# Kernel optimization log

Hardware: AMD Instinct MI355X
Metric: run time of the kernel (lower is better)

Reference implementation:

```python
import jax, jax.numpy as jnp
import numpy as np

B, NV, NH = 65536, 16, 16


def _tri(key, b, n, scale=0.1):
    # well-conditioned lower-triangular 'cholesky-like' factor: unit diagonal + small strict-lower part
    a = jax.random.normal(key, (b, n, n), dtype=jnp.float32) * scale
    return jnp.tril(a, -1) + jnp.eye(n, dtype=jnp.float32)[None, :, :]


def setup_inputs() -> dict:
    key = jax.random.key(0)
    ks = jax.random.split(key, 9)
    # SPD, well-conditioned precision matrix for the hidden block
    a = jax.random.normal(ks[0], (B, NH, NH), dtype=jnp.float32)
    prec_h = jnp.eye(NH, dtype=jnp.float32)[None, :, :] + 0.1 * jnp.matmul(a, jnp.swapaxes(a, -1, -2)) / NH
    return {
        'mu_TE': jax.random.normal(ks[1], (B, NV + NH), dtype=jnp.float32),
        'prec_h': prec_h,
        'chol_v': _tri(ks[2], B, NV),
        'chol_h': _tri(ks[3], B, NH),
        'chol_hv': jax.random.normal(ks[4], (B, NH, NV), dtype=jnp.float32) * 0.1,
        'chol_v_TE': jax.random.normal(ks[5], (B, NV, NV), dtype=jnp.float32) * 0.1,
        'chol_h_TE': jax.random.normal(ks[6], (B, NH, NH), dtype=jnp.float32) * 0.1,
        'chol_hv_TE': jax.random.normal(ks[7], (B, NH, NV), dtype=jnp.float32) * 0.1,
        'chol_amat': _tri(ks[8], B, NV),
        'nv': NV,
    }


def reference(mu_TE, prec_h, chol_v, chol_h, chol_hv, chol_v_TE, chol_h_TE, chol_hv_TE, chol_amat, nv):
    T = lambda m: jnp.swapaxes(m, -1, -2)
    prec_h_inv = jnp.linalg.inv(prec_h)  # [B,nh,nh]

    # d/dt of prec_h_inv via product rule on chol factors
    sym = (chol_h_TE @ T(chol_h) + chol_h @ T(chol_h_TE)
           + chol_hv_TE @ T(chol_hv) + chol_hv @ T(chol_hv_TE))
    prec_h_inv_TE = -(prec_h_inv @ sym @ prec_h_inv)

    # amat_TE = -d/dt [ chol_hv^T prec_h_inv chol_hv ]  -> [B,nv,nv]
    amat_TE = -(T(chol_hv_TE) @ (prec_h_inv @ chol_hv)
                + T(chol_hv) @ (prec_h_inv_TE @ chol_hv)
                + T(chol_hv) @ (prec_h_inv @ chol_hv_TE))

    # make_chol_mat_TE: Phi(L^-1 A L^-T) keeps strict lower triangle + half diagonal
    n = chol_amat.shape[-1]
    phi_mask = jnp.tril(jnp.ones((n, n), jnp.float32), -1) + 0.5 * jnp.eye(n, dtype=jnp.float32)
    cinv = jnp.linalg.inv(chol_amat)
    arg = cinv @ amat_TE @ T(cinv)
    chol_amat_TE = chol_amat @ (arg * phi_mask)

    cholv_TE_std = chol_v_TE @ chol_amat + chol_v @ chol_amat_TE
    muv_TE = mu_TE[:, :nv]
    return cholv_TE_std, muv_TE
```

## Files before the change

kernel.cpp:

```cpp
#include <hip/hip_runtime.h>


typedef _Float16 h2    __attribute__((ext_vector_type(2)));
typedef _Float16 f16x4 __attribute__((ext_vector_type(4)));
typedef float    f32x4 __attribute__((ext_vector_type(4)));

constexpr int PITCH = 20;
constexpr int IMG   = 8 * PITCH;
constexpr int BSTR  = 4 * IMG + 8;

#define WBAR() __builtin_amdgcn_wave_barrier()

__device__ __forceinline__ unsigned int pkf(float a, float b) {
  return __builtin_bit_cast(unsigned int, __builtin_amdgcn_cvt_pkrtz(a, b));
}
__device__ __forceinline__ f16x4 mkf16x4(unsigned int lo, unsigned int hi) {
  union { unsigned int u[2]; f16x4 v; } cv; cv.u[0] = lo; cv.u[1] = hi; return cv.v;
}
__device__ __forceinline__ f16x4 cvt4(f32x4 d) {
  return mkf16x4(pkf(d[0], d[1]), pkf(d[2], d[3]));
}
__device__ __forceinline__ f16x4 cvt4f(float a, float b, float c, float d) {
  return mkf16x4(pkf(a, b), pkf(c, d));
}
__device__ __forceinline__ float dpp_swap1(float v) {
  return __int_as_float(__builtin_amdgcn_update_dpp(
      0, __float_as_int(v), 0xB1, 0xF, 0xF, false));
}
__device__ __forceinline__ f32x4 MF(f16x4 a, f16x4 b, f32x4 c) {
  return __builtin_amdgcn_mfma_f32_16x16x16f16(a, b, c, 0, 0, 0);
}

__device__ __forceinline__ void ldtile(const float* __restrict__ g, size_t batch,
                                       int p, int q, float (&c)[16]) {
  const float* base = g + batch * 256 + p * 64 + q * 4;
  #pragma unroll
  for (int r = 0; r < 4; ++r) {
    float4 v = *reinterpret_cast<const float4*>(base + r * 16);
    c[r*4+0] = v.x; c[r*4+1] = v.y; c[r*4+2] = v.z; c[r*4+3] = v.w;
  }
}
__device__ __forceinline__ void storeRP(unsigned int* img, int p, int q, const float (&c)[16]) {
  #pragma unroll
  for (int r = 0; r < 4; ++r) {
    img[(2*q  ) * PITCH + 4*p + r] = pkf(c[r*4+0], c[r*4+1]);
    img[(2*q+1) * PITCH + 4*p + r] = pkf(c[r*4+2], c[r*4+3]);
  }
}
__device__ __forceinline__ void storeCPt(unsigned int* img, int p, int q, const float (&c)[16]) {
  uint4 w0, w1;
  w0.x = pkf(c[0],  c[4]);  w0.y = pkf(c[1],  c[5]);
  w0.z = pkf(c[2],  c[6]);  w0.w = pkf(c[3],  c[7]);
  w1.x = pkf(c[8],  c[12]); w1.y = pkf(c[9],  c[13]);
  w1.z = pkf(c[10], c[14]); w1.w = pkf(c[11], c[15]);
  *reinterpret_cast<uint4*>(img + (2*p  ) * PITCH + 4*q) = w0;
  *reinterpret_cast<uint4*>(img + (2*p+1) * PITCH + 4*q) = w1;
}

__device__ __forceinline__ f16x4 ldA(const float* __restrict__ X, int r, int h) {
  float4 v = *reinterpret_cast<const float4*>(X + r * 16 + 4 * h);
  return cvt4f(v.x, v.y, v.z, v.w);
}
__device__ __forceinline__ f16x4 ldBcol(const float* __restrict__ X, int h, int c) {
  const float* b = X + 4 * h * 16 + c;
  return cvt4f(b[0], b[16], b[32], b[48]);
}
__device__ __forceinline__ f16x4 ldsB(const unsigned int* img, int h, int c) {
  return mkf16x4(img[(2*h) * PITCH + c], img[(2*h+1) * PITCH + c]);
}
__device__ __forceinline__ f16x4 ldsA(const unsigned int* img, int r, int h) {
  uint4 u = *reinterpret_cast<const uint4*>(img + (r >> 1) * PITCH + 4 * h);
  unsigned int sel = 0x05040100u + (unsigned)(r & 1) * 0x02020202u;
  return mkf16x4(__builtin_amdgcn_perm(u.y, u.x, sel),
                 __builtin_amdgcn_perm(u.w, u.z, sel));
}
__device__ __forceinline__ void stCP(unsigned int* img, int h, int c, f32x4 d) {
  img[(2*h)   * PITCH + c] = pkf(d[0], d[1]);
  img[(2*h+1) * PITCH + c] = pkf(d[2], d[3]);
}

__global__ __launch_bounds__(64, 4) void gauss_te_mf(
    const float* __restrict__ mu_TE,
    const float* __restrict__ prec_h,
    const float* __restrict__ chol_v,
    const float* __restrict__ chol_h,
    const float* __restrict__ chol_hv,
    const float* __restrict__ chol_v_TE,
    const float* __restrict__ chol_h_TE,
    const float* __restrict__ chol_hv_TE,
    const float* __restrict__ chol_amat,
    float* __restrict__ out, int B)
{
  __shared__ __align__(16) unsigned int slab[4 * BSTR];
  const int t = threadIdx.x;
  const int g = t >> 4;
  const int l = t & 15;
  const int p = l >> 2, q = l & 3;
  const size_t batch0 = (size_t)blockIdx.x * 4;
  const size_t tb = batch0 + g;

  unsigned int* Ut  = slab + g * BSTR;
  unsigned int* Q0t = Ut;
  unsigned int* Q1t = Ut + IMG;
  unsigned int* Q2t = Ut + 2 * IMG;
  unsigned int* Q3t = Ut + 3 * IMG;
  float* fcol = reinterpret_cast<float*>(Q3t);
  float* brow = fcol + 32;

  out[(size_t)B * 256 + tb * 16 + l] = mu_TE[tb * 32 + l];

  f16x4 pfA0[4], pfB0[4], pfA1[4], pfB1[4];
  #pragma unroll
  for (int b = 0; b < 4; ++b) {
    const size_t off = (batch0 + b) * 256;
    pfA0[b] = ldA(chol_h_TE  + off, l, g);
    pfB0[b] = ldA(chol_h     + off, l, g);
    pfA1[b] = ldA(chol_hv_TE + off, l, g);
    pfB1[b] = ldA(chol_hv    + off, l, g);
  }

  float la[16];
  ldtile(chol_amat, tb, p, q, la);
  storeCPt(Q1t, p, q, la);
  float pt[16];
  ldtile(prec_h, tb, p, q, pt);
  WBAR();

  #pragma unroll
  for (int k = 0; k < 16; ++k) {
    const int kb = k >> 2, kc = k & 3, sel = (k & 1) * 16;
    if (q == kb) {
      *reinterpret_cast<float4*>(fcol + sel + 4 * p) =
          make_float4(pt[0*4+kc], pt[1*4+kc], pt[2*4+kc], pt[3*4+kc]);
    }
    WBAR();
    if (p == kb) {
      const float rinv = 1.0f / fcol[sel + k];
      float sv[4];
      #pragma unroll
      for (int j = 0; j < 4; ++j) sv[j] = pt[kc*4+j] * rinv;
      if (q == kb) sv[kc] = rinv;
      *reinterpret_cast<float4*>(brow + sel + 4 * q) = make_float4(sv[0], sv[1], sv[2], sv[3]);
    }
    WBAR();
    float4 f4 = *reinterpret_cast<const float4*>(fcol + sel + 4 * p);
    float4 b4 = *reinterpret_cast<const float4*>(brow + sel + 4 * q);
    const float fr[4] = {f4.x, f4.y, f4.z, f4.w};
    const float br[4] = {b4.x, b4.y, b4.z, b4.w};
    #pragma unroll
    for (int r = 0; r < 4; ++r) {
      const bool isPivRow = (p == kb) && (r == kc);
      #pragma unroll
      for (int j = 0; j < 4; ++j) {
        float base = pt[r*4+j];
        if (q == kb && j == kc) base = 0.f;
        const float nv = base - fr[r] * br[j];
        pt[r*4+j] = isPivRow ? br[j] : nv;
      }
    }
  }
  WBAR();
  storeRP(Q0t, p, q, pt);
  WBAR();

  float x[16];
  #pragma unroll
  for (int kp = 0; kp < 8; ++kp) {
    const int r0 = 2 * kp, r1 = r0 + 1;
    float a0 = 0.f, a1 = 0.f, h10 = 0.f;
    #pragma unroll
    for (int c2 = 0; c2 <= kp / 2; ++c2) {
      uint4 cv = *reinterpret_cast<const uint4*>(Q1t + kp * PITCH + 4 * c2);
      const unsigned int cw[4] = {cv.x, cv.y, cv.z, cv.w};
      #pragma unroll
      for (int cc = 0; cc < 4; ++cc) {
        const int j = 4 * c2 + cc;
        h2 hp = __builtin_bit_cast(h2, cw[cc]);
        if (j < r0) a0 = fmaf(-(float)hp.x, x[j], a0);
        if (j < r0) a1 = fmaf(-(float)hp.y, x[j], a1);
        if (j == r0) h10 = (float)hp.y;
      }
    }
    x[r0] = ((l == r0) ? 1.f : 0.f) + a0;
    x[r1] = ((l == r1) ? 1.f : 0.f) + a1 - h10 * x[r0];
  }
  {
    float xp[16];
    #pragma unroll
    for (int j = 0; j < 16; ++j) xp[j] = dpp_swap1(x[j]);
    if ((l & 1) == 0) {
      unsigned int* dst = Q2t + (l >> 1) * PITCH;
      #pragma unroll
      for (int c4 = 0; c4 < 4; ++c4) {
        uint4 w;
        w.x = pkf(x[4*c4+0], xp[4*c4+0]); w.y = pkf(x[4*c4+1], xp[4*c4+1]);
        w.z = pkf(x[4*c4+2], xp[4*c4+2]); w.w = pkf(x[4*c4+3], xp[4*c4+3]);
        *reinterpret_cast<uint4*>(dst + 4*c4) = w;
      }
    }
  }
  WBAR();

  const f32x4 zz = {0.f, 0.f, 0.f, 0.f};
  #pragma unroll
  for (int gb = 0; gb < 4; gb += 2) {
    const unsigned int* Q0[2] = { slab + (gb+0)*BSTR, slab + (gb+1)*BSTR };
    const unsigned int* Q1[2] = { Q0[0] + IMG,        Q0[1] + IMG };
    const unsigned int* Q2[2] = { Q0[0] + 2*IMG,      Q0[1] + 2*IMG };
    unsigned int*       Q3[2] = { slab + (gb+0)*BSTR + 3*IMG,
                                  slab + (gb+1)*BSTR + 3*IMG };
    const size_t off[2] = { (batch0 + gb + 0) * 256, (batch0 + gb + 1) * 256 };

    f16x4 pinvA[2], pinvB[2], hvB[2], cA[2], sumA[2];
    f32x4 W[2], M1[2], Up[2], Zt[2], V2[2];

    #pragma unroll
    for (int u = 0; u < 2; ++u) {
      f32x4 S = MF(pfA0[gb+u], pfB0[gb+u], zz);
      S = MF(pfA1[gb+u], pfB1[gb+u], S);
      pinvA[u] = ldsA(Q0[u], l, g);
      pinvB[u] = ldsB(Q0[u], g, l);
      f32x4 W1 = MF(pinvA[u], cvt4(S), zz);
      stCP(Q3[u], g, l, W1);
    }
    WBAR();
    #pragma unroll
    for (int u = 0; u < 2; ++u) {
      f16x4 w1A = ldsA(Q3[u], l, g);
      W[u] = MF(w1A, pinvB[u], zz);
    }
    #pragma unroll
    for (int u = 0; u < 2; ++u) stCP(Q3[u], g, l, W[u]);
    WBAR();
    #pragma unroll
    for (int u = 0; u < 2; ++u) {
      f16x4 wA = ldsA(Q3[u], l, g);
      sumA[u] = wA + cvt4(W[u]);
      hvB[u] = ldBcol(chol_hv + off[u], g, l);
      M1[u] = MF(pinvA[u], hvB[u], zz);
      Up[u] = MF(sumA[u], hvB[u], zz);
    }
    #pragma unroll
    for (int u = 0; u < 2; ++u) {
      f16x4 hvtB = ldBcol(chol_hv_TE + off[u], g, l);
      Zt[u] = MF(hvtB, cvt4(M1[u]), zz);
      V2[u] = MF(hvB[u], cvt4(Up[u]), zz);
      stCP(Q3[u], g, l, Zt[u]);
    }
    WBAR();
    f32x4 T1[2];
    #pragma unroll
    for (int u = 0; u < 2; ++u) {
      f16x4 zA = ldsA(Q3[u], l, g);
      f32x4 am = V2[u] - Zt[u];
      am[0] -= (float)zA[0]; am[1] -= (float)zA[1];
      am[2] -= (float)zA[2]; am[3] -= (float)zA[3];
      cA[u] = ldsB(Q2[u], g, l);
      T1[u] = MF(cA[u], cvt4(am), zz);
      stCP(Q3[u], g, l, T1[u]);
    }
    WBAR();
    #pragma unroll
    for (int u = 0; u < 2; ++u) {
      f16x4 t1A = ldsA(Q3[u], l, g);
      f32x4 arg = MF(t1A, cA[u], zz);
      #pragma unroll
      for (int j = 0; j < 4; ++j) {
        const int r = 4 * g + j;
        arg[j] = (r > l) ? arg[j] : ((r == l) ? 0.5f * arg[j] : 0.f);
      }
      f32x4 cam = MF(ldA(chol_amat + off[u], l, g), cvt4(arg), zz);
      f16x4 laB = ldsB(Q1[u], g, l);
      f32x4 ov = MF(ldA(chol_v_TE + off[u], l, g), laB, zz);
      ov = MF(ldA(chol_v + off[u], l, g), cvt4(cam), ov);
      float* ob = out + off[u];
      #pragma unroll
      for (int j = 0; j < 4; ++j) ob[(4 * g + j) * 16 + l] = ov[j];
    }
  }
}

extern "C" void kernel_launch(void* const* d_in, const int* in_sizes, int n_in,
                              void* d_out, int out_size, void* d_ws, size_t ws_size,
                              hipStream_t stream) {
  const float* mu_TE      = (const float*)d_in[0];
  const float* prec_h     = (const float*)d_in[1];
  const float* chol_v     = (const float*)d_in[2];
  const float* chol_h     = (const float*)d_in[3];
  const float* chol_hv    = (const float*)d_in[4];
  const float* chol_v_TE  = (const float*)d_in[5];
  const float* chol_h_TE  = (const float*)d_in[6];
  const float* chol_hv_TE = (const float*)d_in[7];
  const float* chol_amat  = (const float*)d_in[8];
  float* out = (float*)d_out;

  const int B = in_sizes[0] / 32;
  gauss_te_mf<<<B / 4, 64, 0, stream>>>(mu_TE, prec_h, chol_v, chol_h, chol_hv,
                                        chol_v_TE, chol_h_TE, chol_hv_TE,
                                        chol_amat, out, B);
}
```

Measured before the change: 126.6 us.

## Use DPP/swizzle Gauss-Jordan pivots and reassociate amat_TE chain to drop LDS round-trips

Result: faster. 122.0 us (-3.6%).

```diff
diff --git a/kernel.cpp b/kernel.cpp
--- a/kernel.cpp
+++ b/kernel.cpp
@@ -7,7 +7,7 @@
 
 constexpr int PITCH = 20;
 constexpr int IMG   = 8 * PITCH;
-constexpr int BSTR  = 4 * IMG + 8;
+constexpr int BSTR  = 3 * IMG + 8;
 
 #define WBAR() __builtin_amdgcn_wave_barrier()
 
@@ -29,6 +29,13 @@
 }
 __device__ __forceinline__ f32x4 MF(f16x4 a, f16x4 b, f32x4 c) {
   return __builtin_amdgcn_mfma_f32_16x16x16f16(a, b, c, 0, 0, 0);
+}
+__device__ __forceinline__ float frcp(float x) {
+#if __has_builtin(__builtin_amdgcn_rcpf)
+  return __builtin_amdgcn_rcpf(x);
+#else
+  return 1.0f / x;
+#endif
 }
 
 __device__ __forceinline__ void ldtile(const float* __restrict__ g, size_t batch,
@@ -79,7 +86,7 @@
   img[(2*h+1) * PITCH + c] = pkf(d[2], d[3]);
 }
 
-__global__ __launch_bounds__(64, 4) void gauss_te_mf(
+__global__ __launch_bounds__(64, 4) void gauss_te_mf2(
     const float* __restrict__ mu_TE,
     const float* __restrict__ prec_h,
     const float* __restrict__ chol_v,
@@ -103,9 +110,6 @@
   unsigned int* Q0t = Ut;
   unsigned int* Q1t = Ut + IMG;
   unsigned int* Q2t = Ut + 2 * IMG;
-  unsigned int* Q3t = Ut + 3 * IMG;
-  float* fcol = reinterpret_cast<float*>(Q3t);
-  float* brow = fcol + 32;
 
   out[(size_t)B * 256 + tb * 16 + l] = mu_TE[tb * 32 + l];
 
@@ -118,49 +122,49 @@
     pfA1[b] = ldA(chol_hv_TE + off, l, g);
     pfB1[b] = ldA(chol_hv    + off, l, g);
   }
+  float pt[16];
+  ldtile(prec_h, tb, p, q, pt);
+
+  #define GJ_STEP(K)                                                          \
+  {                                                                           \
+    constexpr int kb = (K) >> 2, kc = (K) & 3;                                \
+    float F[4];                                                               \
+    _Pragma("unroll")                                                         \
+    for (int r = 0; r < 4; ++r)                                               \
+      F[r] = __int_as_float(__builtin_amdgcn_update_dpp(                      \
+          0, __float_as_int(pt[r*4+kc]), kb * 0x55, 0xF, 0xF, false));        \
+    const float rinv = frcp(F[kc]);                                           \
+    float sv[4];                                                              \
+    _Pragma("unroll")                                                         \
+    for (int j = 0; j < 4; ++j) sv[j] = pt[kc*4+j] * rinv;                    \
+    if (q == kb) sv[kc] = rinv;                                               \
+    float br[4];                                                              \
+    _Pragma("unroll")                                                         \
+    for (int j = 0; j < 4; ++j)                                               \
+      br[j] = __int_as_float(__builtin_amdgcn_ds_swizzle(                     \
+          __float_as_int(sv[j]), ((kb << 2) << 5) | 0x13));                   \
+    _Pragma("unroll")                                                         \
+    for (int r = 0; r < 4; ++r) {                                             \
+      const bool isPivRow = (p == kb) && (r == kc);                           \
+      _Pragma("unroll")                                                       \
+      for (int j = 0; j < 4; ++j) {                                           \
+        float base = pt[r*4+j];                                               \
+        if (q == kb && j == kc) base = 0.f;                                   \
+        const float nv = base - F[r] * br[j];                                 \
+        pt[r*4+j] = isPivRow ? br[j] : nv;                                    \
+      }                                                                       \
+    }                                                                         \
+  }
+  GJ_STEP(0)  GJ_STEP(1)  GJ_STEP(2)  GJ_STEP(3)
+  GJ_STEP(4)  GJ_STEP(5)  GJ_STEP(6)  GJ_STEP(7)
+  GJ_STEP(8)  GJ_STEP(9)  GJ_STEP(10) GJ_STEP(11)
+  GJ_STEP(12) GJ_STEP(13) GJ_STEP(14) GJ_STEP(15)
+  #undef GJ_STEP
+  storeRP(Q0t, p, q, pt);
 
   float la[16];
   ldtile(chol_amat, tb, p, q, la);
   storeCPt(Q1t, p, q, la);
-  float pt[16];
-  ldtile(prec_h, tb, p, q, pt);
-  WBAR();
-
-  #pragma unroll
-  for (int k = 0; k < 16; ++k) {
-    const int kb = k >> 2, kc = k & 3, sel = (k & 1) * 16;
-    if (q == kb) {
-      *reinterpret_cast<float4*>(fcol + sel + 4 * p) =
-          make_float4(pt[0*4+kc], pt[1*4+kc], pt[2*4+kc], pt[3*4+kc]);
-    }
-    WBAR();
-    if (p == kb) {
-      const float rinv = 1.0f / fcol[sel + k];
-      float sv[4];
-      #pragma unroll
-      for (int j = 0; j < 4; ++j) sv[j] = pt[kc*4+j] * rinv;
-      if (q == kb) sv[kc] = rinv;
-      *reinterpret_cast<float4*>(brow + sel + 4 * q) = make_float4(sv[0], sv[1], sv[2], sv[3]);
-    }
-    WBAR();
-    float4 f4 = *reinterpret_cast<const float4*>(fcol + sel + 4 * p);
-    float4 b4 = *reinterpret_cast<const float4*>(brow + sel + 4 * q);
-    const float fr[4] = {f4.x, f4.y, f4.z, f4.w};
-    const float br[4] = {b4.x, b4.y, b4.z, b4.w};
-    #pragma unroll
-    for (int r = 0; r < 4; ++r) {
-      const bool isPivRow = (p == kb) && (r == kc);
-      #pragma unroll
-      for (int j = 0; j < 4; ++j) {
-        float base = pt[r*4+j];
-        if (q == kb && j == kc) base = 0.f;
-        const float nv = base - fr[r] * br[j];
-        pt[r*4+j] = isPivRow ? br[j] : nv;
-      }
-    }
-  }
-  WBAR();
-  storeRP(Q0t, p, q, pt);
   WBAR();
 
   float x[16];
@@ -204,65 +208,43 @@
   const f32x4 zz = {0.f, 0.f, 0.f, 0.f};
   #pragma unroll
   for (int gb = 0; gb < 4; gb += 2) {
-    const unsigned int* Q0[2] = { slab + (gb+0)*BSTR, slab + (gb+1)*BSTR };
-    const unsigned int* Q1[2] = { Q0[0] + IMG,        Q0[1] + IMG };
-    const unsigned int* Q2[2] = { Q0[0] + 2*IMG,      Q0[1] + 2*IMG };
-    unsigned int*       Q3[2] = { slab + (gb+0)*BSTR + 3*IMG,
-                                  slab + (gb+1)*BSTR + 3*IMG };
+    const unsigned int* Q1[2] = { slab + (gb+0)*BSTR + IMG,
+                                  slab + (gb+1)*BSTR + IMG };
+    const unsigned int* Q2[2] = { slab + (gb+0)*BSTR + 2*IMG,
+                                  slab + (gb+1)*BSTR + 2*IMG };
+    unsigned int*       Q0[2] = { slab + (gb+0)*BSTR, slab + (gb+1)*BSTR };
     const size_t off[2] = { (batch0 + gb + 0) * 256, (batch0 + gb + 1) * 256 };
 
-    f16x4 pinvA[2], pinvB[2], hvB[2], cA[2], sumA[2];
-    f32x4 W[2], M1[2], Up[2], Zt[2], V2[2];
-
+    f16x4 pinvF[2], hvB[2], hvtB[2], cA[2];
     #pragma unroll
     for (int u = 0; u < 2; ++u) {
-      f32x4 S = MF(pfA0[gb+u], pfB0[gb+u], zz);
-      S = MF(pfA1[gb+u], pfB1[gb+u], S);
-      pinvA[u] = ldsA(Q0[u], l, g);
-      pinvB[u] = ldsB(Q0[u], g, l);
-      f32x4 W1 = MF(pinvA[u], cvt4(S), zz);
-      stCP(Q3[u], g, l, W1);
+      hvB[u]  = ldBcol(chol_hv + off[u], g, l);
+      hvtB[u] = ldBcol(chol_hv_TE + off[u], g, l);
+      pinvF[u] = ldsA(Q0[u], l, g);
+      cA[u] = ldsB(Q2[u], g, l);
+    }
+    #pragma unroll
+    for (int u = 0; u < 2; ++u) {
+      f32x4 S  = MF(pfA0[gb+u], pfB0[gb+u], zz);
+      S        = MF(pfA1[gb+u], pfB1[gb+u], S);
+      f32x4 St = MF(pfB0[gb+u], pfA0[gb+u], zz);
+      St       = MF(pfB1[gb+u], pfA1[gb+u], St);
+      f32x4 sy = S + St;
+      f32x4 M1 = MF(pinvF[u], hvB[u], zz);
+      f16x4 m1h = cvt4(M1);
+      f32x4 G  = MF(cvt4(sy), m1h, zz);
+      f32x4 Up = MF(pinvF[u], cvt4(G), zz);
+      f32x4 Z  = MF(hvtB[u], m1h, zz);
+      f32x4 ZT = MF(m1h, hvtB[u], zz);
+      f32x4 V2 = MF(hvB[u], cvt4(Up), zz);
+      f32x4 am = V2 - Z - ZT;
+      f32x4 T1 = MF(cA[u], cvt4(am), zz);
+      stCP(Q0[u], g, l, T1);
     }
     WBAR();
     #pragma unroll
     for (int u = 0; u < 2; ++u) {
-      f16x4 w1A = ldsA(Q3[u], l, g);
-      W[u] = MF(w1A, pinvB[u], zz);
-    }
-    #pragma unroll
-    for (int u = 0; u < 2; ++u) stCP(Q3[u], g, l, W[u]);
-    WBAR();
-    #pragma unroll
-    for (int u = 0; u < 2; ++u) {
-      f16x4 wA = ldsA(Q3[u], l, g);
-      sumA[u] = wA + cvt4(W[u]);
-      hvB[u] = ldBcol(chol_hv + off[u], g, l);
-      M1[u] = MF(pinvA[u], hvB[u], zz);
-      Up[u] = MF(sumA[u], hvB[u], zz);
-    }
-    #pragma unroll
-    for (int u = 0; u < 2; ++u) {
-      f16x4 hvtB = ldBcol(chol_hv_TE + off[u], g, l);
-      Zt[u] = MF(hvtB, cvt4(M1[u]), zz);
-      V2[u] = MF(hvB[u], cvt4(Up[u]), zz);
-      stCP(Q3[u], g, l, Zt[u]);
-    }
-    WBAR();
-    f32x4 T1[2];
-    #pragma unroll
-    for (int u = 0; u < 2; ++u) {
-      f16x4 zA = ldsA(Q3[u], l, g);
-      f32x4 am = V2[u] - Zt[u];
-      am[0] -= (float)zA[0]; am[1] -= (float)zA[1];
-      am[2] -= (float)zA[2]; am[3] -= (float)zA[3];
-      cA[u] = ldsB(Q2[u], g, l);
-      T1[u] = MF(cA[u], cvt4(am), zz);
-      stCP(Q3[u], g, l, T1[u]);
-    }
-    WBAR();
-    #pragma unroll
-    for (int u = 0; u < 2; ++u) {
-      f16x4 t1A = ldsA(Q3[u], l, g);
+      f16x4 t1A = ldsA(Q0[u], l, g);
       f32x4 arg = MF(t1A, cA[u], zz);
       #pragma unroll
       for (int j = 0; j < 4; ++j) {
@@ -270,8 +252,7 @@
         arg[j] = (r > l) ? arg[j] : ((r == l) ? 0.5f * arg[j] : 0.f);
       }
       f32x4 cam = MF(ldA(chol_amat + off[u], l, g), cvt4(arg), zz);
-      f16x4 laB = ldsB(Q1[u], g, l);
-      f32x4 ov = MF(ldA(chol_v_TE + off[u], l, g), laB, zz);
+      f32x4 ov = MF(ldA(chol_v_TE + off[u], l, g), ldsB(Q1[u], g, l), zz);
       ov = MF(ldA(chol_v + off[u], l, g), cvt4(cam), ov);
       float* ob = out + off[u];
       #pragma unroll
@@ -295,7 +276,7 @@
   float* out = (float*)d_out;
 
   const int B = in_sizes[0] / 32;
-  gauss_te_mf<<<B / 4, 64, 0, stream>>>(mu_TE, prec_h, chol_v, chol_h, chol_hv,
-                                        chol_v_TE, chol_h_TE, chol_hv_TE,
-                                        chol_amat, out, B);
-}
+  gauss_te_mf2<<<B / 4, 64, 0, stream>>>(mu_TE, prec_h, chol_v, chol_h, chol_hv,
+                                         chol_v_TE, chol_h_TE, chol_hv_TE,
+                                         chol_amat, out, B);
+}
```
